# Performance work log

Hardware: AMD Instinct MI355X
Metric: run time of the kernel (lower is better)

The kernel has to match this reference:

```python
import jax, jax.numpy as jnp
import numpy as np

N_NODES = 100000
F_DIM = 256
NNZ = 1600000  # ~avg degree 16 incidence pairs


def setup_inputs() -> dict:
    key = jax.random.key(0)
    k0, k1, k2, k3 = jax.random.split(key, 4)
    x = jax.random.normal(k0, (N_NODES, F_DIM), dtype=jnp.float32)
    edge_index = jax.random.randint(k1, (2, NNZ), 0, N_NODES, dtype=jnp.int32)
    scale = (2.0 / F_DIM) ** 0.5  # kaiming_normal
    W1 = jax.random.normal(k2, (F_DIM, F_DIM), dtype=jnp.float32) * scale
    W2 = jax.random.normal(k3, (F_DIM, F_DIM), dtype=jnp.float32) * scale
    b1 = jnp.zeros((F_DIM,), jnp.float32)
    b2 = jnp.zeros((F_DIM,), jnp.float32)
    a = jnp.full((1,), 0.25, jnp.float32)  # PReLU shared weight
    return {"x": x, "edge_index": edge_index, "W1": W1, "b1": b1,
            "W2": W2, "b2": b2, "a": a}


def _prelu(x, a):
    return jnp.where(x >= 0, x, a * x)


def _hconv(x, W, b, src, dst, n):
    # PyG HypergraphConv (use_attention=False, edge_weight=1):
    # X' = D^{-1} H B^{-1} H^T X Theta + bias
    xt = x @ W                                   # [N, F]
    ones = jnp.ones(src.shape, xt.dtype)
    D = jax.ops.segment_sum(ones, src, num_segments=n)   # node degree
    B = jax.ops.segment_sum(ones, dst, num_segments=n)   # hyperedge degree
    Dinv = jnp.where(D > 0, 1.0 / D, 0.0)
    Binv = jnp.where(B > 0, 1.0 / B, 0.0)
    # node -> hyperedge: m_e = B^{-1}_e * sum_{i in e} xt_i
    m = jax.ops.segment_sum(xt[src], dst, num_segments=n) * Binv[:, None]
    # hyperedge -> node: out_i = D^{-1}_i * sum_{e ni i} m_e
    out = jax.ops.segment_sum(m[dst], src, num_segments=n) * Dinv[:, None]
    return out + b


def reference(x, edge_index, W1, b1, W2, b2, a):
    src, dst = edge_index[0], edge_index[1]
    n = x.shape[0]  # hyperedge ids are node ids in this module
    h = _prelu(_hconv(x, W1, b1, src, dst, n), a)
    h = _hconv(h, W2, b2, src, dst, n) + x  # residual
    return _prelu(h, a)
```

## Files before the change

### kernel.cpp

```cpp
#include <hip/hip_runtime.h>
#include <hip/hip_bf16.h>


#define F_DIM 256
#define CAP 48
#define BW_SHIFT 9
#define CHUNK 2048

using bf16x8 = __attribute__((ext_vector_type(8))) short;
using f32x4  = __attribute__((ext_vector_type(4))) float;
using half4  = __attribute__((ext_vector_type(4))) _Float16;

__device__ __forceinline__ short f2bf(float f) {
    __hip_bfloat16 h = __float2bfloat16(f);
    return *reinterpret_cast<short*>(&h);
}
__device__ __forceinline__ float bf2f(short s) {
    return __uint_as_float(((unsigned)(unsigned short)s) << 16);
}

__global__ void init_cur_kernel(int* __restrict__ cur, int n, int buckcap) {
    int i = blockIdx.x * blockDim.x + threadIdx.x;
    if (i < n) cur[i] = i * buckcap;
}

__global__ __launch_bounds__(256) void partition_kernel(
    const int* __restrict__ src, const int* __restrict__ dst,
    unsigned* __restrict__ part, int* __restrict__ cur,
    int nnz, int nb, int buckcap)
{
    __shared__ int lhist[256];
    __shared__ int lscan[256];
    __shared__ int gbase[256];
    __shared__ int sh_total;
    __shared__ unsigned lstage[CHUNK];

    const int tid = threadIdx.x;
    const int dir = blockIdx.y;
    const int base = blockIdx.x * CHUNK;
    const int* __restrict__ key = dir ? dst : src;
    const int* __restrict__ val = dir ? src : dst;

    lhist[tid] = 0;
    __syncthreads();

    int myb[8], myr[8];
    unsigned mye[8];
#pragma unroll
    for (int i = 0; i < 8; ++i) {
        int g = base + tid + i * 256;
        myb[i] = -1;
        if (g < nnz) {
            int k = key[g];
            mye[i] = ((unsigned)val[g] << 9) | (unsigned)(k & 511);
            myb[i] = k >> BW_SHIFT;
            myr[i] = atomicAdd(&lhist[myb[i]], 1);
        }
    }
    __syncthreads();

    int v0 = lhist[tid];
    lscan[tid] = v0;
    __syncthreads();
    for (int off = 1; off < 256; off <<= 1) {
        int add = (tid >= off) ? lscan[tid - off] : 0;
        __syncthreads();
        lscan[tid] += add;
        __syncthreads();
    }
    int incl = lscan[tid];
    if (tid == 255) sh_total = incl;
    if (tid < nb && v0 > 0) gbase[tid] = atomicAdd(&cur[dir * nb + tid], v0);
    __syncthreads();
    lscan[tid] = incl - v0;
    __syncthreads();

#pragma unroll
    for (int i = 0; i < 8; ++i)
        if (myb[i] >= 0)
            lstage[lscan[myb[i]] + myr[i]] = (mye[i] & ~0u) | 0u,
            lstage[lscan[myb[i]] + myr[i]] = mye[i];
    __syncthreads();

    const int total = sh_total;
    for (int k = tid; k < total; k += 256) {
        int lo = 0, hi = 255;
        while (lo < hi) {
            int mid = (lo + hi + 1) >> 1;
            if (lscan[mid] <= k) lo = mid; else hi = mid - 1;
        }
        int b = lo;
        int pos = gbase[b] + (k - lscan[b]);
        if (pos < (dir * nb + b + 1) * buckcap)
            part[pos] = lstage[k];
    }
}

__global__ __launch_bounds__(256) void bucket_fill_kernel(
    const unsigned* __restrict__ part, const int* __restrict__ cur,
    int* __restrict__ adjS, int* __restrict__ adjD,
    int* __restrict__ degS, int* __restrict__ degD,
    float* __restrict__ Dinv, float* __restrict__ Binv,
    int M, int nb, int buckcap)
{
    __shared__ int lcnt[512];
    const int tid = threadIdx.x;
    const int b = blockIdx.x;
    const int dir = blockIdx.y;
    const int c = dir * nb + b;
    int* __restrict__ adj = dir ? adjD : adjS;
    int* __restrict__ deg = dir ? degD : degS;
    float* __restrict__ inv = dir ? Binv : Dinv;

    lcnt[tid] = 0;
    lcnt[tid + 256] = 0;
    __syncthreads();

    const int pbase = c * buckcap;
    const int cnt = min(cur[c] - pbase, buckcap);
    const int node0 = b << BW_SHIFT;
    for (int i = tid; i < cnt; i += 256) {
        unsigned e = part[pbase + i];
        int klocal = (int)(e & 511u);
        int v = (int)(e >> 9);
        int r = atomicAdd(&lcnt[klocal], 1);
        if (r < CAP) adj[(size_t)(node0 + klocal) * CAP + r] = v;
    }
    __syncthreads();
    for (int i = tid; i < 512; i += 256) {
        int node = node0 + i;
        if (node < M) {
            int d = min(lcnt[i], CAP);
            deg[node] = d;
            inv[node] = d > 0 ? 1.f / (float)d : 0.f;
        }
    }
}

__global__ void prepack_w_kernel(const float* __restrict__ W,
                                 short* __restrict__ Whi, short* __restrict__ Wlo) {
    int lane = threadIdx.x;
    int nt = blockIdx.x;
    int kt = blockIdx.y;
    int col = nt * 16 + (lane & 15);
    int krow = kt * 32 + (lane >> 4) * 8;
    size_t o = ((size_t)(kt * 16 + nt) * 64 + lane) * 8;
#pragma unroll
    for (int j = 0; j < 8; ++j) {
        float w = W[(size_t)(krow + j) * 256 + col];
        short hi = f2bf(w);
        Whi[o + j] = hi;
        Wlo[o + j] = f2bf(w - bf2f(hi));
    }
}

__global__ __launch_bounds__(256, 2) void gemm_mfma_split(const float* __restrict__ A,
                                                          const short* __restrict__ Whi,
                                                          const short* __restrict__ Wlo,
                                                          _Float16* __restrict__ C, int M) {
    __shared__ short AsHi[4][128][8];
    __shared__ short AsLo[4][128][8];
    const int tid = threadIdx.x;
    const int w = tid >> 6, lane = tid & 63;
    const int quad = lane >> 4, l16 = lane & 15;
    const int bm = blockIdx.x * 128;
    const int wm = (w & 1) * 64;
    const int wnt = (w >> 1) * 8;

    f32x4 acc[4][8] = {};

    for (int kt = 0; kt < 8; ++kt) {
        __syncthreads();
#pragma unroll
        for (int i = 0; i < 2; ++i) {
            int idx = tid + i * 256;
            int row = idx >> 2, seg = idx & 3;
            int grow = bm + row; if (grow >= M) grow = M - 1;
            const float* ap = A + (size_t)grow * 256 + kt * 32 + seg * 8;
            float4 v0 = *(const float4*)ap;
            float4 v1 = *(const float4*)(ap + 4);
            float vv[8] = {v0.x, v0.y, v0.z, v0.w, v1.x, v1.y, v1.z, v1.w};
            union { short s[8]; int4 q; } uh, ul;
#pragma unroll
            for (int e = 0; e < 8; ++e) {
                short hi = f2bf(vv[e]);
                uh.s[e] = hi;
                ul.s[e] = f2bf(vv[e] - bf2f(hi));
            }
            *(int4*)&AsHi[seg][row][0] = uh.q;
            *(int4*)&AsLo[seg][row][0] = ul.q;
        }
        __syncthreads();

        bf16x8 ahi[4], alo[4];
#pragma unroll
        for (int i = 0; i < 4; ++i) {
            ahi[i] = *(const bf16x8*)&AsHi[quad][wm + i * 16 + l16][0];
            alo[i] = *(const bf16x8*)&AsLo[quad][wm + i * 16 + l16][0];
        }

#pragma unroll
        for (int j = 0; j < 8; ++j) {
            int nt = wnt + j;
            size_t off = ((size_t)(kt * 16 + nt) * 64 + lane) * 8;
            bf16x8 bhi = *(const bf16x8*)(Whi + off);
            bf16x8 blo = *(const bf16x8*)(Wlo + off);
#pragma unroll
            for (int i = 0; i < 4; ++i) {
                acc[i][j] = __builtin_amdgcn_mfma_f32_16x16x32_bf16(ahi[i], bhi, acc[i][j], 0, 0, 0);
                acc[i][j] = __builtin_amdgcn_mfma_f32_16x16x32_bf16(ahi[i], blo, acc[i][j], 0, 0, 0);
                acc[i][j] = __builtin_amdgcn_mfma_f32_16x16x32_bf16(alo[i], bhi, acc[i][j], 0, 0, 0);
            }
        }
    }

#pragma unroll
    for (int i = 0; i < 4; ++i) {
#pragma unroll
        for (int j = 0; j < 8; ++j) {
            int col = (wnt + j) * 16 + l16;
            int row0 = bm + wm + i * 16 + quad * 4;
#pragma unroll
            for (int r = 0; r < 4; ++r) {
                int row = row0 + r;
                if (row < M) C[(size_t)row * 256 + col] = (_Float16)acc[i][j][r];
            }
        }
    }
}

template <int OUT_F16>
__global__ __launch_bounds__(256) void gather_rows_kernel(const _Float16* __restrict__ src_mat,
                                                          void* __restrict__ out_mat,
                                                          const int* __restrict__ deg,
                                                          const int* __restrict__ adj,
                                                          const float* __restrict__ scale,
                                                          const float* __restrict__ bias,
                                                          const float* __restrict__ residual,
                                                          const float* __restrict__ alpha_p,
                                                          int n) {
    int wid = (blockIdx.x * blockDim.x + threadIdx.x) >> 6;
    int lane = threadIdx.x & 63;
    if (wid >= n) return;
    const int dcount = deg[wid];
    const int* arow = adj + (size_t)wid * CAP;
    int myidx = (lane < dcount) ? __builtin_nontemporal_load(arow + lane) : 0;

    const size_t lo = (size_t)lane * 4;
    float a0 = 0.f, a1 = 0.f, a2 = 0.f, a3 = 0.f;

    for (int j = 0; j < dcount; ++j) {
        int idx = __shfl(myidx, j);
        half4 v = *(const half4*)(src_mat + (size_t)idx * F_DIM + lo);
        a0 += (float)v.x; a1 += (float)v.y; a2 += (float)v.z; a3 += (float)v.w;
    }

    float sc = scale[wid];
    a0 *= sc; a1 *= sc; a2 *= sc; a3 *= sc;
    if (bias) {
        float4 bb = ((const float4*)bias)[lane];
        a0 += bb.x; a1 += bb.y; a2 += bb.z; a3 += bb.w;
    }
    if (residual) {
        const float* rp = residual + (size_t)wid * F_DIM + lo;
        float4 xv;
        xv.x = __builtin_nontemporal_load(rp + 0);
        xv.y = __builtin_nontemporal_load(rp + 1);
        xv.z = __builtin_nontemporal_load(rp + 2);
        xv.w = __builtin_nontemporal_load(rp + 3);
        a0 += xv.x; a1 += xv.y; a2 += xv.z; a3 += xv.w;
    }
    if (alpha_p) {
        float al = alpha_p[0];
        a0 = a0 >= 0.f ? a0 : al * a0;
        a1 = a1 >= 0.f ? a1 : al * a1;
        a2 = a2 >= 0.f ? a2 : al * a2;
        a3 = a3 >= 0.f ? a3 : al * a3;
    }
    if (OUT_F16) {
        half4 o;
        o.x = (_Float16)a0; o.y = (_Float16)a1; o.z = (_Float16)a2; o.w = (_Float16)a3;
        *(half4*)((_Float16*)out_mat + (size_t)wid * F_DIM + lo) = o;
    } else {
        float4 o = make_float4(a0, a1, a2, a3);
        *(float4*)((float*)out_mat + (size_t)wid * F_DIM + lo) = o;
    }
}

extern "C" void kernel_launch(void* const* d_in, const int* in_sizes, int n_in,
                              void* d_out, int out_size, void* d_ws, size_t ws_size,
                              hipStream_t stream) {
    const float* x   = (const float*)d_in[0];
    const int*   ei  = (const int*)d_in[1];
    const float* W1  = (const float*)d_in[2];
    const float* b1  = (const float*)d_in[3];
    const float* W2  = (const float*)d_in[4];
    const float* b2  = (const float*)d_in[5];
    const float* a   = (const float*)d_in[6];
    float* out = (float*)d_out;

    const int M   = in_sizes[0] / F_DIM;
    const int nnz = in_sizes[1] / 2;
    const int* src = ei;
    const int* dst = ei + nnz;

    const int NB = (M + (1 << BW_SHIFT) - 1) >> BW_SHIFT;
    const int avg = (int)(((long long)nnz << BW_SHIFT) / M);
    const int BUCKCAP = avg + avg / 8 + 256;
    const int nchunks = (nnz + CHUNK - 1) / CHUNK;

    char* p = (char*)d_ws;
    const size_t nbuf   = (size_t)M * F_DIM * sizeof(float);
    const size_t nbuf16 = (size_t)M * F_DIM * sizeof(_Float16);
    const size_t wpk    = 8 * 16 * 64 * 8 * sizeof(short);
    float*    bufH  = (float*)p;           p += nbuf;
    _Float16* bufXT = (_Float16*)p;        p += nbuf16;
    _Float16* bufM  = (_Float16*)p;        p += nbuf16;
    short* W1hi = (short*)p;               p += wpk;
    short* W1lo = (short*)p;               p += wpk;
    short* W2hi = (short*)p;               p += wpk;
    short* W2lo = (short*)p;               p += wpk;
    int* adjS   = (int*)p;                 p += (size_t)M * CAP * 4;
    int* adjD   = (int*)p;                 p += (size_t)M * CAP * 4;
    int* degS   = (int*)p;                 p += (size_t)M * 4;
    int* degD   = (int*)p;                 p += (size_t)M * 4;
    float* Dinv = (float*)p;               p += (size_t)M * 4;
    float* Binv = (float*)p;               p += (size_t)M * 4;
    int* bucketCur = (int*)p;              p += ((size_t)2 * NB * 4 + 15) & ~15ull;

    unsigned* part = (unsigned*)bufH;

    const dim3 blk(256);
    const dim3 gemm_grid((M + 127) / 128);
    const int gather_blocks = (M + 3) / 4;

    init_cur_kernel<<<(2 * NB + 255) / 256, blk, 0, stream>>>(bucketCur, 2 * NB, BUCKCAP);
    partition_kernel<<<dim3(nchunks, 2), blk, 0, stream>>>(src, dst, part, bucketCur,
                                                           nnz, NB, BUCKCAP);
    bucket_fill_kernel<<<dim3(NB, 2), blk, 0, stream>>>(part, bucketCur, adjS, adjD,
                                                        degS, degD, Dinv, Binv,
                                                        M, NB, BUCKCAP);

    prepack_w_kernel<<<dim3(16, 8), 64, 0, stream>>>(W1, W1hi, W1lo);
    prepack_w_kernel<<<dim3(16, 8), 64, 0, stream>>>(W2, W2hi, W2lo);

    gemm_mfma_split<<<gemm_grid, blk, 0, stream>>>(x, W1hi, W1lo, bufXT, M);
    gather_rows_kernel<1><<<gather_blocks, blk, 0, stream>>>(bufXT, bufM, degD, adjD,
                                                             Binv, nullptr, nullptr, nullptr, M);
    gather_rows_kernel<0><<<gather_blocks, blk, 0, stream>>>(bufM, bufH, degS, adjS,
                                                             Dinv, b1, nullptr, a, M);
    gemm_mfma_split<<<gemm_grid, blk, 0, stream>>>(bufH, W2hi, W2lo, bufXT, M);
    gather_rows_kernel<1><<<gather_blocks, blk, 0, stream>>>(bufXT, bufM, degD, adjD,
                                                             Binv, nullptr, nullptr, nullptr, M);
    gather_rows_kernel<0><<<gather_blocks, blk, 0, stream>>>(bufM, out, degS, adjS,
                                                             Dinv, b2, x, a, M);
}
```

Measured before the change: 917.0 us.

## Drop LDS staging in GEMM, store hidden in fp16, skip partition binary search

The GEMM no longer stages A through shared memory. Each wave loads its A fragments straight from global memory and splits them into bf16 hi/lo registers, and the grid is split into two column halves with smaller accumulator tiles. The intermediate hidden activation is now written as fp16 instead of fp32, which halves the traffic for the second GEMM's input. The partition kernel stores each element's bucket id in shared memory so it can drop the per-element binary search over the scan. The risks are duplicated A reads across column blocks and the lower precision of fp16 for the hidden activation.

```diff
diff --git a/kernel.cpp b/kernel.cpp
--- a/kernel.cpp
+++ b/kernel.cpp
@@ -10,6 +10,7 @@
 using bf16x8 = __attribute__((ext_vector_type(8))) short;
 using f32x4  = __attribute__((ext_vector_type(4))) float;
 using half4  = __attribute__((ext_vector_type(4))) _Float16;
+using half8  = __attribute__((ext_vector_type(8))) _Float16;
 
 __device__ __forceinline__ short f2bf(float f) {
     __hip_bfloat16 h = __float2bfloat16(f);
@@ -34,6 +35,7 @@
     __shared__ int gbase[256];
     __shared__ int sh_total;
     __shared__ unsigned lstage[CHUNK];
+    __shared__ unsigned char lbuck[CHUNK];
 
     const int tid = threadIdx.x;
     const int dir = blockIdx.y;
@@ -77,19 +79,16 @@
 
 #pragma unroll
     for (int i = 0; i < 8; ++i)
-        if (myb[i] >= 0)
-            lstage[lscan[myb[i]] + myr[i]] = (mye[i] & ~0u) | 0u,
-            lstage[lscan[myb[i]] + myr[i]] = mye[i];
+        if (myb[i] >= 0) {
+            int pos = lscan[myb[i]] + myr[i];
+            lstage[pos] = mye[i];
+            lbuck[pos] = (unsigned char)myb[i];
+        }
     __syncthreads();
 
     const int total = sh_total;
     for (int k = tid; k < total; k += 256) {
-        int lo = 0, hi = 255;
-        while (lo < hi) {
-            int mid = (lo + hi + 1) >> 1;
-            if (lscan[mid] <= k) lo = mid; else hi = mid - 1;
-        }
-        int b = lo;
+        int b = lbuck[k];
         int pos = gbase[b] + (k - lscan[b]);
         if (pos < (dir * nb + b + 1) * buckcap)
             part[pos] = lstage[k];
@@ -154,54 +153,51 @@
     }
 }
 
-__global__ __launch_bounds__(256, 2) void gemm_mfma_split(const float* __restrict__ A,
-                                                          const short* __restrict__ Whi,
-                                                          const short* __restrict__ Wlo,
-                                                          _Float16* __restrict__ C, int M) {
-    __shared__ short AsHi[4][128][8];
-    __shared__ short AsLo[4][128][8];
+template <typename AT>
+__global__ __launch_bounds__(256) void gemm_direct(const AT* __restrict__ A,
+                                                   const short* __restrict__ Whi,
+                                                   const short* __restrict__ Wlo,
+                                                   _Float16* __restrict__ C, int M) {
     const int tid = threadIdx.x;
     const int w = tid >> 6, lane = tid & 63;
     const int quad = lane >> 4, l16 = lane & 15;
     const int bm = blockIdx.x * 128;
+    const int bn_t = blockIdx.y * 8;
     const int wm = (w & 1) * 64;
-    const int wnt = (w >> 1) * 8;
-
-    f32x4 acc[4][8] = {};
-
+    const int wnt = (w >> 1) * 4;
+
+    f32x4 acc[4][4] = {};
+
+#pragma unroll
     for (int kt = 0; kt < 8; ++kt) {
-        __syncthreads();
-#pragma unroll
-        for (int i = 0; i < 2; ++i) {
-            int idx = tid + i * 256;
-            int row = idx >> 2, seg = idx & 3;
-            int grow = bm + row; if (grow >= M) grow = M - 1;
-            const float* ap = A + (size_t)grow * 256 + kt * 32 + seg * 8;
-            float4 v0 = *(const float4*)ap;
-            float4 v1 = *(const float4*)(ap + 4);
-            float vv[8] = {v0.x, v0.y, v0.z, v0.w, v1.x, v1.y, v1.z, v1.w};
-            union { short s[8]; int4 q; } uh, ul;
+        bf16x8 ahi[4], alo[4];
+#pragma unroll
+        for (int i = 0; i < 4; ++i) {
+            int row = bm + wm + i * 16 + l16;
+            if (row >= M) row = M - 1;
+            const AT* ap = A + (size_t)row * 256 + kt * 32 + quad * 8;
+            float vv[8];
+            if constexpr (sizeof(AT) == 4) {
+                float4 v0 = *(const float4*)ap;
+                float4 v1 = *(const float4*)(ap + 4);
+                vv[0] = v0.x; vv[1] = v0.y; vv[2] = v0.z; vv[3] = v0.w;
+                vv[4] = v1.x; vv[5] = v1.y; vv[6] = v1.z; vv[7] = v1.w;
+            } else {
+                half8 v = *(const half8*)ap;
+#pragma unroll
+                for (int e = 0; e < 8; ++e) vv[e] = (float)v[e];
+            }
 #pragma unroll
             for (int e = 0; e < 8; ++e) {
                 short hi = f2bf(vv[e]);
-                uh.s[e] = hi;
-                ul.s[e] = f2bf(vv[e] - bf2f(hi));
+                ahi[i][e] = hi;
+                alo[i][e] = f2bf(vv[e] - bf2f(hi));
             }
-            *(int4*)&AsHi[seg][row][0] = uh.q;
-            *(int4*)&AsLo[seg][row][0] = ul.q;
-        }
-        __syncthreads();
-
-        bf16x8 ahi[4], alo[4];
-#pragma unroll
-        for (int i = 0; i < 4; ++i) {
-            ahi[i] = *(const bf16x8*)&AsHi[quad][wm + i * 16 + l16][0];
-            alo[i] = *(const bf16x8*)&AsLo[quad][wm + i * 16 + l16][0];
-        }
-
-#pragma unroll
-        for (int j = 0; j < 8; ++j) {
-            int nt = wnt + j;
+        }
+
+#pragma unroll
+        for (int j = 0; j < 4; ++j) {
+            int nt = bn_t + wnt + j;
             size_t off = ((size_t)(kt * 16 + nt) * 64 + lane) * 8;
             bf16x8 bhi = *(const bf16x8*)(Whi + off);
             bf16x8 blo = *(const bf16x8*)(Wlo + off);
@@ -217,8 +213,8 @@
 #pragma unroll
     for (int i = 0; i < 4; ++i) {
 #pragma unroll
-        for (int j = 0; j < 8; ++j) {
-            int col = (wnt + j) * 16 + l16;
+        for (int j = 0; j < 4; ++j) {
+            int col = (bn_t + wnt + j) * 16 + l16;
             int row0 = bm + wm + i * 16 + quad * 4;
 #pragma unroll
             for (int r = 0; r < 4; ++r) {
@@ -313,7 +309,7 @@
     const size_t nbuf   = (size_t)M * F_DIM * sizeof(float);
     const size_t nbuf16 = (size_t)M * F_DIM * sizeof(_Float16);
     const size_t wpk    = 8 * 16 * 64 * 8 * sizeof(short);
-    float*    bufH  = (float*)p;           p += nbuf;
+    _Float16* bufH  = (_Float16*)p;        p += nbuf;
     _Float16* bufXT = (_Float16*)p;        p += nbuf16;
     _Float16* bufM  = (_Float16*)p;        p += nbuf16;
     short* W1hi = (short*)p;               p += wpk;
@@ -331,7 +327,7 @@
     unsigned* part = (unsigned*)bufH;
 
     const dim3 blk(256);
-    const dim3 gemm_grid((M + 127) / 128);
+    const dim3 gemm_grid((M + 127) / 128, 2);
     const int gather_blocks = (M + 3) / 4;
 
     init_cur_kernel<<<(2 * NB + 255) / 256, blk, 0, stream>>>(bucketCur, 2 * NB, BUCKCAP);
@@ -344,12 +340,12 @@
     prepack_w_kernel<<<dim3(16, 8), 64, 0, stream>>>(W1, W1hi, W1lo);
     prepack_w_kernel<<<dim3(16, 8), 64, 0, stream>>>(W2, W2hi, W2lo);
 
-    gemm_mfma_split<<<gemm_grid, blk, 0, stream>>>(x, W1hi, W1lo, bufXT, M);
+    gemm_direct<float><<<gemm_grid, blk, 0, stream>>>(x, W1hi, W1lo, bufXT, M);
     gather_rows_kernel<1><<<gather_blocks, blk, 0, stream>>>(bufXT, bufM, degD, adjD,
                                                              Binv, nullptr, nullptr, nullptr, M);
-    gather_rows_kernel<0><<<gather_blocks, blk, 0, stream>>>(bufM, bufH, degS, adjS,
+    gather_rows_kernel<1><<<gather_blocks, blk, 0, stream>>>(bufM, bufH, degS, adjS,
                                                              Dinv, b1, nullptr, a, M);
-    gemm_mfma_split<<<gemm_grid, blk, 0, stream>>>(bufH, W2hi, W2lo, bufXT, M);
+    gemm_direct<_Float16><<<gemm_grid, blk, 0, stream>>>(bufH, W2hi, W2lo, bufXT, M);
     gather_rows_kernel<1><<<gather_blocks, blk, 0, stream>>>(bufXT, bufM, degD, adjD,
                                                              Binv, nullptr, nullptr, nullptr, M);
     gather_rows_kernel<0><<<gather_blocks, blk, 0, stream>>>(bufM, out, degS, adjS,
```

New measurement: 900.9 us. No clear change (-1.8%).
